# Performance work log

Hardware: AMD Instinct MI355X
Metric: run time of the kernel (lower is better)

## Reference

```python
import jax, jax.numpy as jnp
import numpy as np

N = 100_000   # nodes
E = 1_600_000 # edges
C = 64        # in = hidden = out channels
H = 8         # heads
D = C // H    # head_dim = 8
R = 4         # relations
L = 2         # layers


def setup_inputs() -> dict:
    key = jax.random.key(0)
    ks = jax.random.split(key, 10)
    sc = 1.0 / np.sqrt(C)  # xavier-ish scale
    return {
        "x": jax.random.normal(ks[0], (N, C), jnp.float32),
        "edge_index": jax.random.randint(ks[1], (2, E), 0, N),
        "edge_type": jax.random.randint(ks[2], (E,), 0, R),
        "W_Q": jax.random.normal(ks[3], (L, R, H, C, D), jnp.float32) * sc,
        "W_K": jax.random.normal(ks[4], (L, R, H, C, D), jnp.float32) * sc,
        "W_V": jax.random.normal(ks[5], (L, R, H, C, D), jnp.float32) * sc,
        "W_concat": jax.random.normal(ks[6], (L, R, H * D, C), jnp.float32) * sc,
        "sem_w": jax.random.normal(ks[7], (L, C), jnp.float32) * sc,
        "sem_b": jnp.zeros((L,), jnp.float32),
        "W_self": jax.random.normal(ks[8], (L, C, C), jnp.float32) * sc,
        "ln_g": jnp.ones((L, C), jnp.float32),
        "ln_b": jnp.zeros((L, C), jnp.float32),
    }


def _layer(x, src, dst, edge_type, WQ, WK, WV, Wcat, sw, sb, Ws, g, b):
    inv_sqrt_d = 1.0 / np.sqrt(D)
    rel_msgs = []
    for r in range(R):  # small fixed relation loop
        mask = (edge_type == r).astype(x.dtype)             # (E,)
        Q = jnp.einsum('nc,hcd->nhd', x, WQ[r])             # (N,H,D)
        K = jnp.einsum('nc,hcd->nhd', x, WK[r])
        V = jnp.einsum('nc,hcd->nhd', x, WV[r])
        # edge-wise QK energy, leaky_relu(0.01), scatter-add into dst node
        energy = jnp.einsum('ehd,ehd->eh', Q[dst], K[src]) * inv_sqrt_d
        energy = jax.nn.leaky_relu(energy)                  # (E,H)
        alpha_n = jax.ops.segment_sum(energy * mask[:, None], dst,
                                      num_segments=N)       # (N,H)
        alpha = jax.nn.softmax(alpha_n, axis=0)             # softmax over nodes
        w = alpha[dst] * mask[:, None]                      # (E,H)
        m = jax.ops.segment_sum(w[:, :, None] * V[src], dst,
                                num_segments=N)             # (N,H,D)
        rel_msgs.append(m.reshape(N, H * D) @ Wcat[r])      # (N,C)
    stacked = jnp.stack(rel_msgs)                           # (R,N,C)
    beta = jax.nn.softmax(stacked @ sw + sb, axis=0)        # (R,N) semantic attn
    agg = jnp.einsum('rn,rnc->nc', beta, stacked)           # (N,C)
    y = x + jax.nn.gelu(x @ Ws + agg, approximate=False)
    mu = y.mean(-1, keepdims=True)
    var = y.var(-1, keepdims=True)
    return (y - mu) / jnp.sqrt(var + 1e-5) * g + b


def reference(x, edge_index, edge_type, W_Q, W_K, W_V, W_concat,
              sem_w, sem_b, W_self, ln_g, ln_b):
    src, dst = edge_index[0], edge_index[1]  # PyG source_to_target: j=row0, i=row1
    for l in range(L):
        x = _layer(x, src, dst, edge_type, W_Q[l], W_K[l], W_V[l], W_concat[l],
                   sem_w[l], sem_b[l], W_self[l], ln_g[l], ln_b[l])
        # inter-layer dropout omitted (inference / eval mode)
    return x
```

## Files before the change

### kernel.cpp

```cpp
#include <hip/hip_runtime.h>
#include <hip/hip_bf16.h>

#define NN 100000
#define EE 1600000
#define RRR 4
#define HHH 8
#define NT 400000
#define GG 782
#define SHIFT 9
#define NBLK 512
#define CHUNK 3125
#define BMAX 2560

typedef unsigned int u32;
typedef unsigned short u16;
typedef __attribute__((ext_vector_type(8))) short bf16x8;
typedef __attribute__((ext_vector_type(4))) float f32x4;

static constexpr size_t OFF_KV   = 0;
static constexpr size_t OFF_Q    = 102400000;
static constexpr size_t OFF_S    = 153600000;
static constexpr size_t OFF_AL   = 217600000;
static constexpr size_t OFF_PW   = 230400000;
static constexpr size_t OFF_PART = 230700000;
static constexpr size_t OFF_FIN  = 230710000;
static constexpr size_t OFF_CW   = 230720000;
static constexpr size_t OFF_ROWP = 232400000;
static constexpr size_t OFF_EDG  = 234100000;
static constexpr size_t OFF_BSTORE = OFF_S;
static constexpr size_t OFF_HIST   = OFF_S + 8000000;
static constexpr size_t OFF_OFFA   = OFF_S + 16000000;
static constexpr size_t OFF_BASE   = OFF_S + 24000000;

__device__ inline u16 f2bf(float f){
  union { __hip_bfloat16 h; u16 u; } cv; cv.h = __float2bfloat16(f); return cv.u;
}
__device__ inline float bf2f(u16 u){ return __uint_as_float(((u32)u) << 16); }

__global__ __launch_bounds__(256) void k_histA(const int* __restrict__ dst, const int* __restrict__ typ,
                                               u32* __restrict__ Hist){
  __shared__ u32 h[GG];
  int b = blockIdx.x, t = threadIdx.x;
  for (int g = t; g < GG; g += 256) h[g] = 0u;
  __syncthreads();
  int e0 = b * CHUNK;
  for (int e = e0 + t; e < e0 + CHUNK; e += 256){
    int seg = typ[e] * NN + dst[e];
    atomicAdd(&h[seg >> SHIFT], 1u);
  }
  __syncthreads();
  for (int g = t; g < GG; g += 256) Hist[(size_t)b * GG + g] = h[g];
}

__global__ __launch_bounds__(1024) void k_base(const u32* __restrict__ Hist, u32* __restrict__ Base,
                                               u32* __restrict__ rowp){
  __shared__ u32 tot[GG];
  int t = threadIdx.x;
  if (t < GG){
    u32 s = 0;
    for (int b = 0; b < NBLK; b++) s += Hist[(size_t)b * GG + t];
    tot[t] = s;
  }
  __syncthreads();
  if (t == 0){
    u32 acc = 0;
    for (int g = 0; g < GG; g++){ u32 c = tot[g]; Base[g] = acc; acc += c; }
    Base[GG] = acc;
    rowp[NT] = EE;
  }
}

__global__ __launch_bounds__(512) void k_off(const u32* __restrict__ Hist, const u32* __restrict__ Base,
                                             u32* __restrict__ Off){
  __shared__ u32 v[NBLK];
  int g = blockIdx.x, t = threadIdx.x;
  v[t] = Hist[(size_t)t * GG + g];
  __syncthreads();
  if (t == 0){
    u32 acc = Base[g];
    for (int b = 0; b < NBLK; b++){ u32 c = v[b]; v[b] = acc; acc += c; }
  }
  __syncthreads();
  Off[(size_t)g * NBLK + t] = v[t];
}

__global__ __launch_bounds__(256) void k_fill(const int* __restrict__ src, const int* __restrict__ dst,
                                              const int* __restrict__ typ, const u32* __restrict__ Off,
                                              u32* __restrict__ bstore){
  __shared__ u32 cur[GG];
  int b = blockIdx.x, t = threadIdx.x;
  for (int g = t; g < GG; g += 256) cur[g] = Off[(size_t)g * NBLK + b];
  __syncthreads();
  int e0 = b * CHUNK;
  for (int e = e0 + t; e < e0 + CHUNK; e += 256){
    int seg = typ[e] * NN + dst[e];
    u32 pos = atomicAdd(&cur[seg >> SHIFT], 1u);
    bstore[pos] = ((u32)(seg & 511) << 17) | (u32)src[e];
  }
}

__global__ __launch_bounds__(256) void k_sortD(const u32* __restrict__ bstore, const u32* __restrict__ Base,
                                               u32* __restrict__ rowp, u32* __restrict__ edges){
  __shared__ u32 ent[BMAX];
  __shared__ u32 binc[512], bexc[512];
  int g = blockIdx.x, t = threadIdx.x;
  u32 base = Base[g];
  u32 cnt = Base[g + 1] - base;
  if (cnt > (u32)BMAX) cnt = (u32)BMAX;
  for (int i = t; i < 512; i += 256) binc[i] = 0u;
  __syncthreads();
  for (u32 i = t; i < cnt; i += 256){
    u32 v = bstore[base + i];
    ent[i] = v;
    atomicAdd(&binc[v >> 17], 1u);
  }
  __syncthreads();
  if (t == 0){
    u32 acc = 0;
    #pragma unroll 8
    for (int s = 0; s < 512; s++){ u32 c = binc[s]; bexc[s] = acc; binc[s] = acc; acc += c; }
  }
  __syncthreads();
  for (int s = t; s < 512; s += 256){
    int seg = g * 512 + s;
    if (seg < NT) rowp[seg] = base + bexc[s];
  }
  __syncthreads();
  for (u32 i = t; i < cnt; i += 256){
    u32 v = ent[i];
    u32 p = atomicAdd(&binc[v >> 17], 1u);
    edges[base + p] = v & 0x1FFFFu;
  }
}

__global__ __launch_bounds__(256) void k_repackbf(const float* __restrict__ WQ, const float* __restrict__ WK,
                                                  const float* __restrict__ WV, const float* __restrict__ Wcat,
                                                  const float* __restrict__ Wself, u16* __restrict__ pwB){
  int t = blockIdx.x * 256 + threadIdx.x;
  if (t >= 2 * 17 * 4096) return;
  int l = t / (17 * 4096), rem = t % (17 * 4096);
  int mat = rem >> 12, idx = rem & 4095;
  int out = idx >> 6, c = idx & 63;
  float v;
  if (mat < 12){
    int kind = mat >> 2, r = mat & 3;
    int h = out >> 3, d = out & 7;
    const float* Wsrc = (kind == 0) ? WQ : (kind == 1) ? WK : WV;
    v = Wsrc[((((l * RRR + r) * HHH + h) * 64) + c) * 8 + d];
  } else if (mat == 12){
    v = Wself[(l * 64 + c) * 64 + out];
  } else {
    int r = mat - 13;
    v = Wcat[(((l * RRR + r) * 64) + c) * 64 + out];
  }
  pwB[t] = f2bf(v);
}

__global__ __launch_bounds__(512) void k_cw(const float* __restrict__ Wcat, const float* __restrict__ semw,
                                            float* __restrict__ cw){
  int t = threadIdx.x;
  int l = t >> 8, r = (t >> 6) & 3, k = t & 63;
  const float* wp = Wcat + (((size_t)(l * RRR + r) * 64) + k) * 64;
  const float* sp = semw + l * 64;
  float s = 0.f;
  #pragma unroll 8
  for (int c = 0; c < 64; c++) s += wp[c] * sp[c];
  cw[t] = s;
}


__global__ __launch_bounds__(256) void k_qkvself(const float* __restrict__ x, const u16* __restrict__ pwL,
                                                 u16* __restrict__ QAll, u32* __restrict__ kvpAll){
  __shared__ u16 xa[64][72];
  int t = threadIdx.x;
  int n0 = blockIdx.x * 64;
  {
    int row = t >> 2, c0 = (t & 3) * 16;
    int n = n0 + row;
    float4 v0 = {}, v1 = {}, v2 = {}, v3 = {};
    if (n < NN){
      const float4* xp = (const float4*)(x + (size_t)n * 64 + c0);
      v0 = xp[0]; v1 = xp[1]; v2 = xp[2]; v3 = xp[3];
    }
    ushort4* dp = (ushort4*)&xa[row][c0];
    dp[0] = make_ushort4(f2bf(v0.x), f2bf(v0.y), f2bf(v0.z), f2bf(v0.w));
    dp[1] = make_ushort4(f2bf(v1.x), f2bf(v1.y), f2bf(v1.z), f2bf(v1.w));
    dp[2] = make_ushort4(f2bf(v2.x), f2bf(v2.y), f2bf(v2.z), f2bf(v2.w));
    dp[3] = make_ushort4(f2bf(v3.x), f2bf(v3.y), f2bf(v3.z), f2bf(v3.w));
  }
  __syncthreads();
  int w = t >> 6, lane = t & 63;
  int ra = w * 16 + (lane & 15);
  int kg = (lane >> 4) * 8;
  int cb = lane & 15;
  int rb = (lane >> 4) * 4;
  bf16x8 a0 = *(const bf16x8*)&xa[ra][kg];
  bf16x8 a1 = *(const bf16x8*)&xa[ra][32 + kg];
  f32x4 z = {0.f, 0.f, 0.f, 0.f};
  #pragma unroll
  for (int m = 0; m < 4; m++){
    const u16* wp = pwL + (size_t)m * 4096;
    f32x4 acc[4] = {z, z, z, z};
    #pragma unroll
    for (int t4 = 0; t4 < 4; t4++){
      bf16x8 b0 = *(const bf16x8*)(wp + (t4 * 16 + cb) * 64 + kg);
      bf16x8 b1 = *(const bf16x8*)(wp + (t4 * 16 + cb) * 64 + 32 + kg);
      acc[t4] = __builtin_amdgcn_mfma_f32_16x16x32_bf16(a0, b0, acc[t4], 0, 0, 0);
      acc[t4] = __builtin_amdgcn_mfma_f32_16x16x32_bf16(a1, b1, acc[t4], 0, 0, 0);
    }
    u16* op = QAll + (size_t)m * NN * 64;
    #pragma unroll
    for (int t4 = 0; t4 < 4; t4++){
      #pragma unroll
      for (int i2 = 0; i2 < 4; i2++){
        int n = n0 + w * 16 + rb + i2;
        if (n < NN) op[(size_t)n * 64 + t4 * 16 + cb] = f2bf(acc[t4][i2]);
      }
    }
  }
  #pragma unroll
  for (int r = 0; r < 4; r++){
    const u16* wk = pwL + (size_t)(4 + r) * 4096;
    const u16* wv = pwL + (size_t)(8 + r) * 4096;
    f32x4 ak[4] = {z, z, z, z};
    f32x4 av[4] = {z, z, z, z};
    #pragma unroll
    for (int t4 = 0; t4 < 4; t4++){
      bf16x8 bk0 = *(const bf16x8*)(wk + (t4 * 16 + cb) * 64 + kg);
      bf16x8 bk1 = *(const bf16x8*)(wk + (t4 * 16 + cb) * 64 + 32 + kg);
      bf16x8 bv0 = *(const bf16x8*)(wv + (t4 * 16 + cb) * 64 + kg);
      bf16x8 bv1 = *(const bf16x8*)(wv + (t4 * 16 + cb) * 64 + 32 + kg);
      ak[t4] = __builtin_amdgcn_mfma_f32_16x16x32_bf16(a0, bk0, ak[t4], 0, 0, 0);
      ak[t4] = __builtin_amdgcn_mfma_f32_16x16x32_bf16(a1, bk1, ak[t4], 0, 0, 0);
      av[t4] = __builtin_amdgcn_mfma_f32_16x16x32_bf16(a0, bv0, av[t4], 0, 0, 0);
      av[t4] = __builtin_amdgcn_mfma_f32_16x16x32_bf16(a1, bv1, av[t4], 0, 0, 0);
    }
    u32* kp = kvpAll + (size_t)r * NN * 64;
    #pragma unroll
    for (int t4 = 0; t4 < 4; t4++){
      #pragma unroll
      for (int i2 = 0; i2 < 4; i2++){
        int n = n0 + w * 16 + rb + i2;
        if (n < NN) kp[(size_t)n * 64 + t4 * 16 + cb] = (u32)f2bf(ak[t4][i2]) | ((u32)f2bf(av[t4][i2]) << 16);
      }
    }
  }
}

__global__ __launch_bounds__(256) void k_gather4(const u32* __restrict__ edges, const u32* __restrict__ rowp,
                                                 const u32* __restrict__ kvpAll, const u16* __restrict__ QAll,
                                                 u16* __restrict__ Sb, float* __restrict__ alphaB){
  int wid = threadIdx.x >> 6, lane = threadIdx.x & 63;
  int qt = lane >> 4;
  int i  = lane & 15;
  int n = blockIdx.x * 4 + wid;
  const float isd = 0.35355339059327373f;
  #pragma unroll
  for (int r = 0; r < 4; r++){
    const u32* kvp = kvpAll + (size_t)r * NN * 64;
    ushort4 qv = *(const ushort4*)&QAll[((size_t)r * NN + n) * 64 + 4 * i];
    float q0 = bf2f(qv.x), q1 = bf2f(qv.y), q2 = bf2f(qv.z), q3 = bf2f(qv.w);
    u32 beg = rowp[(size_t)r * NN + n], end = rowp[(size_t)r * NN + n + 1];
    float sx = 0.f, sy = 0.f, sz = 0.f, sw = 0.f, aa = 0.f;
    for (u32 base = beg; base < end; base += 64){
      u32 cnt = (end - base < 64u) ? (end - base) : 64u;
      u32 eidx = (base + (u32)lane < end) ? edges[base + lane] : 0u;
      for (u32 j = 0; j < cnt; j += 4){
        u32 jj = j + (u32)qt;
        float mk = (jj < cnt) ? 1.f : 0.f;
        u32 js = (jj < cnt) ? jj : (cnt - 1);
        int s = __shfl((int)eidx, (int)js);
        uint4 w = *(const uint4*)&kvp[(size_t)s * 64 + 4 * i];
        float p = q0 * bf2f((u16)(w.x & 0xFFFFu)) + q1 * bf2f((u16)(w.y & 0xFFFFu))
                + q2 * bf2f((u16)(w.z & 0xFFFFu)) + q3 * bf2f((u16)(w.w & 0xFFFFu));
        p += __shfl_xor(p, 1);
        float e = p * isd;
        e = (e > 0.f) ? e : 0.01f * e;
        aa += e * mk;
        sx += bf2f((u16)(w.x >> 16)) * mk;
        sy += bf2f((u16)(w.y >> 16)) * mk;
        sz += bf2f((u16)(w.z >> 16)) * mk;
        sw += bf2f((u16)(w.w >> 16)) * mk;
      }
    }
    sx += __shfl_xor(sx, 16); sx += __shfl_xor(sx, 32);
    sy += __shfl_xor(sy, 16); sy += __shfl_xor(sy, 32);
    sz += __shfl_xor(sz, 16); sz += __shfl_xor(sz, 32);
    sw += __shfl_xor(sw, 16); sw += __shfl_xor(sw, 32);
    aa += __shfl_xor(aa, 16); aa += __shfl_xor(aa, 32);
    if (qt == 0){
      ushort4 o; o.x = f2bf(sx); o.y = f2bf(sy); o.z = f2bf(sz); o.w = f2bf(sw);
      *(ushort4*)&Sb[((size_t)r * NN + n) * 64 + 4 * i] = o;
      if ((i & 1) == 0) alphaB[((size_t)r * NN + n) * 8 + (i >> 1)] = aa;
    }
  }
}

__global__ __launch_bounds__(256) void k_stats1(const float* __restrict__ alpha, float2* __restrict__ part){
  int r = blockIdx.y;
  int chunk = blockIdx.x;
  const int per = (NN + 31) / 32;
  int nbeg = chunk * per;
  int nend = nbeg + per; if (nend > NN) nend = NN;
  int t = threadIdx.x;
  int h = t & 7;
  int g = t >> 3;
  float m = -1e30f, s = 0.f;
  for (int n = nbeg + g; n < nend; n += 32){
    float a = alpha[((size_t)r * NN + n) * 8 + h];
    if (a > m){ s *= expf(m - a); m = a; }
    s += expf(a - m);
  }
  __shared__ float sm[256], ss[256];
  sm[t] = m; ss[t] = s; __syncthreads();
  for (int off = 128; off >= 8; off >>= 1){
    if (t < off){
      float m2 = sm[t + off], s2 = ss[t + off];
      float M = fmaxf(sm[t], m2);
      ss[t] = ss[t] * expf(sm[t] - M) + s2 * expf(m2 - M);
      sm[t] = M;
    }
    __syncthreads();
  }
  if (t < 8) part[(r * 8 + t) * 32 + chunk] = make_float2(sm[t], ss[t]);
}

__global__ void k_stats2(const float2* __restrict__ part, float2* __restrict__ fin){
  int col = threadIdx.x;
  if (col < 32){
    float M = -1e30f, S = 0.f;
    for (int i = 0; i < 32; i++){
      float2 p = part[col * 32 + i];
      float Mn = fmaxf(M, p.x);
      S = S * expf(M - Mn) + p.y * expf(p.x - Mn);
      M = Mn;
    }
    fin[col] = make_float2(M, 1.f / S);
  }
}

__global__ __launch_bounds__(256) void k_msgfin(const u16* __restrict__ S, const float* __restrict__ alpha,
                                                const float2* __restrict__ fin, const u16* __restrict__ pwL,
                                                const float* __restrict__ cwL, const float* __restrict__ xin,
                                                const float* __restrict__ lng, const float* __restrict__ lnb,
                                                float* __restrict__ xout){
  __shared__ u16 As[4][64][72];
  __shared__ u16 xa[64][72];
  __shared__ float lgs[4][64];
  __shared__ float beta[4][64];
  int t = threadIdx.x;
  int n0 = blockIdx.x * 64;
  {
    int row = t >> 2, c0 = (t & 3) * 16;
    int n = n0 + row;
    float4 v0 = {}, v1 = {}, v2 = {}, v3 = {};
    if (n < NN){
      const float4* xp = (const float4*)(xin + (size_t)n * 64 + c0);
      v0 = xp[0]; v1 = xp[1]; v2 = xp[2]; v3 = xp[3];
    }
    ushort4* dp = (ushort4*)&xa[row][c0];
    dp[0] = make_ushort4(f2bf(v0.x), f2bf(v0.y), f2bf(v0.z), f2bf(v0.w));
    dp[1] = make_ushort4(f2bf(v1.x), f2bf(v1.y), f2bf(v1.z), f2bf(v1.w));
    dp[2] = make_ushort4(f2bf(v2.x), f2bf(v2.y), f2bf(v2.z), f2bf(v2.w));
    dp[3] = make_ushort4(f2bf(v3.x), f2bf(v3.y), f2bf(v3.z), f2bf(v3.w));
  }
  #pragma unroll
  for (int r = 0; r < 4; r++){
    int row = t >> 2, c0 = (t & 3) * 16;
    int n = n0 + row;
    int na = (n < NN) ? n : (NN - 1);
    int h0 = c0 >> 3;
    float2 f0 = fin[r * 8 + h0];
    float2 f1 = fin[r * 8 + h0 + 1];
    float a0 = alpha[((size_t)r * NN + na) * 8 + h0];
    float a1 = alpha[((size_t)r * NN + na) * 8 + h0 + 1];
    float w0 = expf(a0 - f0.x) * f0.y;
    float w1 = expf(a1 - f1.x) * f1.y;
    const u32* sp = (const u32*)(S + ((size_t)r * NN + na) * 64 + c0);
    const float* cwr = cwL + r * 64;
    float lgp = 0.f;
    #pragma unroll
    for (int jj = 0; jj < 8; jj++){
      u32 bts = sp[jj];
      float wm = (jj < 4) ? w0 : w1;
      float mv0 = bf2f((u16)(bts & 0xFFFFu)) * wm;
      float mv1 = bf2f((u16)(bts >> 16)) * wm;
      lgp += mv0 * cwr[c0 + jj * 2] + mv1 * cwr[c0 + jj * 2 + 1];
      ushort2 o;
      o.x = f2bf(mv0);
      o.y = f2bf(mv1);
      *(ushort2*)&As[r][row][c0 + jj * 2] = o;
    }
    lgp += __shfl_xor(lgp, 1);
    lgp += __shfl_xor(lgp, 2);
    if ((t & 3) == 0) lgs[r][row] = lgp;
  }
  __syncthreads();
  if (t < 64){
    float l0 = lgs[0][t], l1 = lgs[1][t], l2 = lgs[2][t], l3 = lgs[3][t];
    float mx = fmaxf(fmaxf(l0, l1), fmaxf(l2, l3));
    float e0 = expf(l0 - mx), e1 = expf(l1 - mx), e2 = expf(l2 - mx), e3 = expf(l3 - mx);
    float inv = 1.f / (e0 + e1 + e2 + e3);
    beta[0][t] = e0 * inv; beta[1][t] = e1 * inv; beta[2][t] = e2 * inv; beta[3][t] = e3 * inv;
  }
  __syncthreads();
  int w = t >> 6, lane = t & 63;
  int ra = w * 16 + (lane & 15);
  int kg = (lane >> 4) * 8;
  int cb = lane & 15;
  int rb = (lane >> 4) * 4;
  f32x4 z = {0.f, 0.f, 0.f, 0.f};
  f32x4 agg[4] = {z, z, z, z};
  #pragma unroll
  for (int r = 0; r < 4; r++){
    bf16x8 a0 = *(const bf16x8*)&As[r][ra][kg];
    bf16x8 a1 = *(const bf16x8*)&As[r][ra][32 + kg];
    const u16* wp = pwL + (size_t)(13 + r) * 4096;
    float br[4];
    #pragma unroll
    for (int i2 = 0; i2 < 4; i2++) br[i2] = beta[r][w * 16 + rb + i2];
    #pragma unroll
    for (int t4 = 0; t4 < 4; t4++){
      f32x4 acc = z;
      bf16x8 b0 = *(const bf16x8*)(wp + (t4 * 16 + cb) * 64 + kg);
      bf16x8 b1 = *(const bf16x8*)(wp + (t4 * 16 + cb) * 64 + 32 + kg);
      acc = __builtin_amdgcn_mfma_f32_16x16x32_bf16(a0, b0, acc, 0, 0, 0);
      acc = __builtin_amdgcn_mfma_f32_16x16x32_bf16(a1, b1, acc, 0, 0, 0);
      #pragma unroll
      for (int i2 = 0; i2 < 4; i2++) agg[t4][i2] += br[i2] * acc[i2];
    }
  }
  {
    bf16x8 a0 = *(const bf16x8*)&xa[ra][kg];
    bf16x8 a1 = *(const bf16x8*)&xa[ra][32 + kg];
    const u16* wp = pwL + (size_t)12 * 4096;
    #pragma unroll
    for (int t4 = 0; t4 < 4; t4++){
      f32x4 acc = z;
      bf16x8 b0 = *(const bf16x8*)(wp + (t4 * 16 + cb) * 64 + kg);
      bf16x8 b1 = *(const bf16x8*)(wp + (t4 * 16 + cb) * 64 + 32 + kg);
      acc = __builtin_amdgcn_mfma_f32_16x16x32_bf16(a0, b0, acc, 0, 0, 0);
      acc = __builtin_amdgcn_mfma_f32_16x16x32_bf16(a1, b1, acc, 0, 0, 0);
      agg[t4] += acc;
    }
  }
  float ys[4][4];
  #pragma unroll
  for (int t4 = 0; t4 < 4; t4++){
    #pragma unroll
    for (int i2 = 0; i2 < 4; i2++){
      int n = n0 + w * 16 + rb + i2;
      int ch = t4 * 16 + cb;
      float pre = agg[t4][i2];
      float ge = 0.5f * pre * (1.f + erff(pre * 0.70710678118654752f));
      float xv = (n < NN) ? xin[(size_t)n * 64 + ch] : 0.f;
      ys[t4][i2] = xv + ge;
    }
  }
  float mu[4], rs[4];
  #pragma unroll
  for (int i2 = 0; i2 < 4; i2++){
    float s = (ys[0][i2] + ys[1][i2]) + (ys[2][i2] + ys[3][i2]);
    s += __shfl_xor(s, 1); s += __shfl_xor(s, 2); s += __shfl_xor(s, 4); s += __shfl_xor(s, 8);
    mu[i2] = s * (1.f / 64.f);
  }
  #pragma unroll
  for (int i2 = 0; i2 < 4; i2++){
    float d0 = ys[0][i2] - mu[i2], d1 = ys[1][i2] - mu[i2];
    float d2 = ys[2][i2] - mu[i2], d3 = ys[3][i2] - mu[i2];
    float v = (d0 * d0 + d1 * d1) + (d2 * d2 + d3 * d3);
    v += __shfl_xor(v, 1); v += __shfl_xor(v, 2); v += __shfl_xor(v, 4); v += __shfl_xor(v, 8);
    rs[i2] = rsqrtf(v * (1.f / 64.f) + 1e-5f);
  }
  #pragma unroll
  for (int t4 = 0; t4 < 4; t4++){
    #pragma unroll
    for (int i2 = 0; i2 < 4; i2++){
      int n = n0 + w * 16 + rb + i2;
      int ch = t4 * 16 + cb;
      if (n < NN) xout[(size_t)n * 64 + ch] = (ys[t4][i2] - mu[i2]) * rs[i2] * lng[ch] + lnb[ch];
    }
  }
}

extern "C" void kernel_launch(void* const* d_in, const int* in_sizes, int n_in,
                              void* d_out, int out_size, void* d_ws, size_t ws_size,
                              hipStream_t stream){
  const float* x0    = (const float*)d_in[0];
  const int*   eidx  = (const int*)d_in[1];
  const int*   etyp  = (const int*)d_in[2];
  const float* WQ    = (const float*)d_in[3];
  const float* WK    = (const float*)d_in[4];
  const float* WV    = (const float*)d_in[5];
  const float* Wcat  = (const float*)d_in[6];
  const float* semw  = (const float*)d_in[7];
  const float* semb  = (const float*)d_in[8];
  const float* Wself = (const float*)d_in[9];
  const float* lng   = (const float*)d_in[10];
  const float* lnb   = (const float*)d_in[11];
  float* out = (float*)d_out;
  char* ws = (char*)d_ws;

  const int* srcArr = eidx;
  const int* dstArr = eidx + EE;

  u32*  kvpAll   = (u32*)(ws + OFF_KV);
  u16*  Qb       = (u16*)(ws + OFF_Q);
  u16*  Sb       = (u16*)(ws + OFF_S);
  float* alphaB  = (float*)(ws + OFF_AL);
  u16*  pwB      = (u16*)(ws + OFF_PW);
  float2* part   = (float2*)(ws + OFF_PART);
  float2* fin    = (float2*)(ws + OFF_FIN);
  float* cw      = (float*)(ws + OFF_CW);
  u32* rowp   = (u32*)(ws + OFF_ROWP);
  u32* edges  = (u32*)(ws + OFF_EDG);
  u32* bstore = (u32*)(ws + OFF_BSTORE);
  u32* Hist   = (u32*)(ws + OFF_HIST);
  u32* Off    = (u32*)(ws + OFF_OFFA);
  u32* Base   = (u32*)(ws + OFF_BASE);

  k_histA<<<NBLK, 256, 0, stream>>>(dstArr, etyp, Hist);
  k_base<<<1, 1024, 0, stream>>>(Hist, Base, rowp);
  k_off<<<GG, 512, 0, stream>>>(Hist, Base, Off);
  k_fill<<<NBLK, 256, 0, stream>>>(srcArr, dstArr, etyp, Off, bstore);
  k_sortD<<<GG, 256, 0, stream>>>(bstore, Base, rowp, edges);
  k_repackbf<<<(2 * 17 * 4096 + 255) / 256, 256, 0, stream>>>(WQ, WK, WV, Wcat, Wself, pwB);
  k_cw<<<1, 512, 0, stream>>>(Wcat, semw, cw);

  for (int l = 0; l < 2; l++){
    const float* xcur = (l == 0) ? x0 : out;
    const u16* pwL = pwB + (size_t)l * 17 * 4096;
    k_qkvself<<<1563, 256, 0, stream>>>(xcur, pwL, Qb, kvpAll);
    k_gather4<<<NN / 4, 256, 0, stream>>>(edges, rowp, kvpAll, Qb, Sb, alphaB);
    k_stats1<<<dim3(32, 4), 256, 0, stream>>>(alphaB, part);
    k_stats2<<<1, 64, 0, stream>>>(part, fin);
    k_msgfin<<<1563, 256, 0, stream>>>(Sb, alphaB, fin, pwL, cw + l * 256, xcur,
                                       lng + l * 64, lnb + l * 64, out);
  }
  (void)in_sizes; (void)n_in; (void)out_size; (void)ws_size;
  (void)semb;
}
```

Baseline: 722.1 us.

## Interleave four relation edge walks in gather kernel to overlap gathers

The gather kernel used to walk each relation's CSR edge list one after another. It now walks all four relations' edge lists at once, one wave per node, and issues four independent K/V row loads per iteration so more memory requests are in flight. This is meant to hide gather latency. In exchange it uses more registers per thread, and iterations are wasted on masked lanes when the four relations have very different degrees.

```diff
diff --git a/kernel.cpp b/kernel.cpp
--- a/kernel.cpp
+++ b/kernel.cpp
@@ -255,43 +255,68 @@
   int i  = lane & 15;
   int n = blockIdx.x * 4 + wid;
   const float isd = 0.35355339059327373f;
+  u32 beg[4], end[4], cur[4], wb[4], eidx[4];
+  float q0[4], q1[4], q2[4], q3[4];
   #pragma unroll
   for (int r = 0; r < 4; r++){
-    const u32* kvp = kvpAll + (size_t)r * NN * 64;
+    beg[r] = rowp[(size_t)r * NN + n];
+    end[r] = rowp[(size_t)r * NN + n + 1];
+    cur[r] = beg[r]; wb[r] = beg[r];
+    eidx[r] = (beg[r] + (u32)lane < end[r]) ? edges[beg[r] + lane] : 0u;
     ushort4 qv = *(const ushort4*)&QAll[((size_t)r * NN + n) * 64 + 4 * i];
-    float q0 = bf2f(qv.x), q1 = bf2f(qv.y), q2 = bf2f(qv.z), q3 = bf2f(qv.w);
-    u32 beg = rowp[(size_t)r * NN + n], end = rowp[(size_t)r * NN + n + 1];
-    float sx = 0.f, sy = 0.f, sz = 0.f, sw = 0.f, aa = 0.f;
-    for (u32 base = beg; base < end; base += 64){
-      u32 cnt = (end - base < 64u) ? (end - base) : 64u;
-      u32 eidx = (base + (u32)lane < end) ? edges[base + lane] : 0u;
-      for (u32 j = 0; j < cnt; j += 4){
-        u32 jj = j + (u32)qt;
-        float mk = (jj < cnt) ? 1.f : 0.f;
-        u32 js = (jj < cnt) ? jj : (cnt - 1);
-        int s = __shfl((int)eidx, (int)js);
-        uint4 w = *(const uint4*)&kvp[(size_t)s * 64 + 4 * i];
-        float p = q0 * bf2f((u16)(w.x & 0xFFFFu)) + q1 * bf2f((u16)(w.y & 0xFFFFu))
-                + q2 * bf2f((u16)(w.z & 0xFFFFu)) + q3 * bf2f((u16)(w.w & 0xFFFFu));
-        p += __shfl_xor(p, 1);
-        float e = p * isd;
-        e = (e > 0.f) ? e : 0.01f * e;
-        aa += e * mk;
-        sx += bf2f((u16)(w.x >> 16)) * mk;
-        sy += bf2f((u16)(w.y >> 16)) * mk;
-        sz += bf2f((u16)(w.z >> 16)) * mk;
-        sw += bf2f((u16)(w.w >> 16)) * mk;
+    q0[r] = bf2f(qv.x); q1[r] = bf2f(qv.y); q2[r] = bf2f(qv.z); q3[r] = bf2f(qv.w);
+  }
+  float sx[4] = {0.f,0.f,0.f,0.f}, sy[4] = {0.f,0.f,0.f,0.f};
+  float sz[4] = {0.f,0.f,0.f,0.f}, sw[4] = {0.f,0.f,0.f,0.f};
+  float aa[4] = {0.f,0.f,0.f,0.f};
+  while ((cur[0] < end[0]) | (cur[1] < end[1]) | (cur[2] < end[2]) | (cur[3] < end[3])){
+    u32 s[4];
+    float mk[4];
+    #pragma unroll
+    for (int r = 0; r < 4; r++){
+      if (cur[r] - wb[r] >= 64u && cur[r] < end[r]){
+        wb[r] = cur[r];
+        eidx[r] = (wb[r] + (u32)lane < end[r]) ? edges[wb[r] + lane] : 0u;
       }
-    }
-    sx += __shfl_xor(sx, 16); sx += __shfl_xor(sx, 32);
-    sy += __shfl_xor(sy, 16); sy += __shfl_xor(sy, 32);
-    sz += __shfl_xor(sz, 16); sz += __shfl_xor(sz, 32);
-    sw += __shfl_xor(sw, 16); sw += __shfl_xor(sw, 32);
-    aa += __shfl_xor(aa, 16); aa += __shfl_xor(aa, 32);
+      u32 wcnt = end[r] - wb[r]; if (wcnt > 64u) wcnt = 64u;
+      u32 jj = cur[r] - wb[r] + (u32)qt;
+      bool act = (cur[r] < end[r]) && (jj < wcnt);
+      mk[r] = act ? 1.f : 0.f;
+      u32 js = (jj < wcnt) ? jj : (wcnt ? wcnt - 1u : 0u);
+      s[r] = (u32)__shfl((int)eidx[r], (int)js);
+    }
+    uint4 w0 = *(const uint4*)&kvpAll[(size_t)s[0] * 64 + 4 * i];
+    uint4 w1 = *(const uint4*)&kvpAll[(size_t)NN * 64 + (size_t)s[1] * 64 + 4 * i];
+    uint4 w2 = *(const uint4*)&kvpAll[(size_t)2 * NN * 64 + (size_t)s[2] * 64 + 4 * i];
+    uint4 w3 = *(const uint4*)&kvpAll[(size_t)3 * NN * 64 + (size_t)s[3] * 64 + 4 * i];
+    #pragma unroll
+    for (int r = 0; r < 4; r++){
+      uint4 w = (r == 0) ? w0 : (r == 1) ? w1 : (r == 2) ? w2 : w3;
+      float p = q0[r] * bf2f((u16)(w.x & 0xFFFFu)) + q1[r] * bf2f((u16)(w.y & 0xFFFFu))
+              + q2[r] * bf2f((u16)(w.z & 0xFFFFu)) + q3[r] * bf2f((u16)(w.w & 0xFFFFu));
+      p += __shfl_xor(p, 1);
+      float e = p * isd;
+      e = (e > 0.f) ? e : 0.01f * e;
+      aa[r] += e * mk[r];
+      sx[r] += bf2f((u16)(w.x >> 16)) * mk[r];
+      sy[r] += bf2f((u16)(w.y >> 16)) * mk[r];
+      sz[r] += bf2f((u16)(w.z >> 16)) * mk[r];
+      sw[r] += bf2f((u16)(w.w >> 16)) * mk[r];
+      cur[r] += 4;
+      if (cur[r] > end[r]) cur[r] = end[r];
+    }
+  }
+  #pragma unroll
+  for (int r = 0; r < 4; r++){
+    sx[r] += __shfl_xor(sx[r], 16); sx[r] += __shfl_xor(sx[r], 32);
+    sy[r] += __shfl_xor(sy[r], 16); sy[r] += __shfl_xor(sy[r], 32);
+    sz[r] += __shfl_xor(sz[r], 16); sz[r] += __shfl_xor(sz[r], 32);
+    sw[r] += __shfl_xor(sw[r], 16); sw[r] += __shfl_xor(sw[r], 32);
+    aa[r] += __shfl_xor(aa[r], 16); aa[r] += __shfl_xor(aa[r], 32);
     if (qt == 0){
-      ushort4 o; o.x = f2bf(sx); o.y = f2bf(sy); o.z = f2bf(sz); o.w = f2bf(sw);
+      ushort4 o; o.x = f2bf(sx[r]); o.y = f2bf(sy[r]); o.z = f2bf(sz[r]); o.w = f2bf(sw[r]);
       *(ushort4*)&Sb[((size_t)r * NN + n) * 64 + 4 * i] = o;
-      if ((i & 1) == 0) alphaB[((size_t)r * NN + n) * 8 + (i >> 1)] = aa;
+      if ((i & 1) == 0) alphaB[((size_t)r * NN + n) * 8 + (i >> 1)] = aa[r];
     }
   }
 }
```

Result: slower. 760.3 us (+5.3%).
